# Kernel tuning notes

Hardware: AMD Instinct MI355X
Metric: run time of the kernel (lower is better)

## Reference

```python
import jax, jax.numpy as jnp
import numpy as np
from jax import lax

B, C, H, W = 4, 256, 64, 64
M = 8
CP = C // M  # 32 attention channels
KS = (3, 5, 7, 9)
EPS = 1e-5


def conv1x1(a, w, b):
    # a: [B,Ci,H,W], w: [Co,Ci], b: [Co]
    return jnp.einsum('bchw,oc->bohw', a, w) + b[None, :, None, None]


def _patches(a, k):
    # im2col with padding k//2, stride 1 (matches torch.nn.Unfold(k,1,k//2,1))
    pad = k // 2
    p = lax.conv_general_dilated_patches(a, (k, k), (1, 1), [(pad, pad), (pad, pad)])
    Bb, Cc = a.shape[0], a.shape[1]
    return p.reshape(Bb, Cc, k * k, a.shape[2], a.shape[3])  # [B,C',k^2,H,W]


def local_attn(km, qm, xm, k):
    # query is the center of each patch == qm itself (stride 1, pad k//2)
    kp = _patches(km, k)                                   # [B,C',k^2,H,W]
    scores = jnp.einsum('bckhw,bchw->bkhw', kp, qm)        # per-pixel k^2 logits
    attn = jax.nn.softmax(scores, axis=1)                  # softmax over window (dim=-2 in torch)
    xp = _patches(xm, k)                                   # [B,C',k^2,H,W]
    return jnp.einsum('bckhw,bkhw->bchw', xp, attn)        # [B,C',H,W]


def setup_inputs() -> dict:
    key = jax.random.key(0)
    ks = jax.random.split(key, 12)
    s_in = 1.0 / np.sqrt(C)
    s_out = 1.0 / np.sqrt(CP)
    return {
        'x': jax.random.normal(ks[0], (B, C, H, W), jnp.float32),
        'vessel': jax.random.uniform(ks[1], (B, 1, H, W), jnp.float32),
        'wk': jax.random.normal(ks[2], (CP, C), jnp.float32) * s_in,
        'bk': jnp.zeros((CP,), jnp.float32),
        'wq': jax.random.normal(ks[3], (CP, C), jnp.float32) * s_in,
        'bq': jnp.zeros((CP,), jnp.float32),
        'wx': jax.random.normal(ks[4], (CP, C), jnp.float32) * s_in,
        'bx': jnp.zeros((CP,), jnp.float32),
        'wf': jax.random.normal(ks[5], (C, CP), jnp.float32) * s_out,
        'bf': jnp.zeros((C,), jnp.float32),
        'gamma': jnp.ones((C,), jnp.float32),
        'beta': jnp.zeros((C,), jnp.float32),
    }


def reference(x, vessel, wk, bk, wq, bq, wx, bx, wf, bf, gamma, beta):
    km = conv1x1(x, wk, bk) * vessel   # key map masked by vessel
    qm = conv1x1(x, wq, bq)            # query map
    xm = conv1x1(x, wx, bx)            # value map
    pre = local_attn(km, qm, xm, KS[0])
    for k in KS[1:]:
        pre = pre + local_attn(km, qm, xm, k)
    y = conv1x1(pre, wf, bf)           # [B,C,H,W]
    # BatchNorm2d (training-mode batch stats)
    mean = y.mean(axis=(0, 2, 3), keepdims=True)
    var = y.var(axis=(0, 2, 3), keepdims=True)
    yn = (y - mean) * lax.rsqrt(var + EPS)
    return x + gamma[None, :, None, None] * yn + beta[None, :, None, None]
```

## Files before the change

### kernel.cpp

```cpp
#include <hip/hip_runtime.h>
#include <hip/hip_bf16.h>

typedef __hip_bfloat16 bf16;
typedef unsigned short u16;
typedef unsigned int u32;

typedef __bf16 bf16x8 __attribute__((ext_vector_type(8)));
typedef float f32x4 __attribute__((ext_vector_type(4)));

__device__ __forceinline__ float bf2f(bf16 v) { return __bfloat162float(v); }
__device__ __forceinline__ float us2f(u16 u) {
    union { u32 i; float f; } c; c.i = ((u32)u) << 16; return c.f;
}
__device__ __forceinline__ u16 f2u(float f) {
    union { bf16 b; u16 u; } c; c.b = __float2bfloat16(f); return c.u;
}

__global__ __launch_bounds__(256) void k_proj(
    const float* __restrict__ x, const float* __restrict__ vessel,
    const float* __restrict__ wk, const float* __restrict__ bk,
    const float* __restrict__ wq, const float* __restrict__ bq,
    const float* __restrict__ wx, const float* __restrict__ bx,
    bf16* __restrict__ km, bf16* __restrict__ qm, bf16* __restrict__ xm,
    float* __restrict__ partials)
{
    __shared__ u16 xs[64 * 264];
    __shared__ u16 wsh[48 * 264];
    const int tid = threadIdx.x;
    const int bid = blockIdx.x;
    const int nh = bid & 1;
    const int pt = bid >> 1;
    const int b  = pt >> 6;
    const int p0 = (pt & 63) * 64;

    if (bid < 64) {
#pragma unroll
        for (int i = 0; i < 5; ++i) {
            const int idx = tid + i * 256;
            if (idx < 1056) partials[bid * 1056 + idx] = 0.f;
        }
    }

#pragma unroll
    for (int i = 0; i < 16; ++i) {
        const int idx4 = tid + i * 256;
        const int ch = idx4 >> 4;
        const int px4 = (idx4 & 15) * 4;
        const float4 v = *(const float4*)&x[(b * 256 + ch) * 4096 + p0 + px4];
        xs[(px4 + 0) * 264 + ch] = f2u(v.x);
        xs[(px4 + 1) * 264 + ch] = f2u(v.y);
        xs[(px4 + 2) * 264 + ch] = f2u(v.z);
        xs[(px4 + 3) * 264 + ch] = f2u(v.w);
    }
#pragma unroll
    for (int i = 0; i < 12; ++i) {
        const int idx4 = tid + i * 256;
        const int o = idx4 >> 6;
        const int ch4 = (idx4 & 63) * 4;
        const int go = nh * 48 + o;
        const float* wp = (go < 32) ? wk : ((go < 64) ? wq : wx);
        const float4 v = *(const float4*)&wp[(go & 31) * 256 + ch4];
        wsh[o * 264 + ch4 + 0] = f2u(v.x);
        wsh[o * 264 + ch4 + 1] = f2u(v.y);
        wsh[o * 264 + ch4 + 2] = f2u(v.z);
        wsh[o * 264 + ch4 + 3] = f2u(v.w);
    }
    __syncthreads();

    const int w = tid >> 6;
    const int lane = tid & 63;
    const int lm = lane & 15, quad = lane >> 4;

    f32x4 acc0 = {0.f, 0.f, 0.f, 0.f};
    f32x4 acc1 = {0.f, 0.f, 0.f, 0.f};
    f32x4 acc2 = {0.f, 0.f, 0.f, 0.f};
#pragma unroll
    for (int kk = 0; kk < 8; ++kk) {
        const int k0 = kk * 32 + quad * 8;
        const bf16x8 a  = *(const bf16x8*)&xs[(w * 16 + lm) * 264 + k0];
        const bf16x8 b0 = *(const bf16x8*)&wsh[(0 + lm) * 264 + k0];
        const bf16x8 b1 = *(const bf16x8*)&wsh[(16 + lm) * 264 + k0];
        const bf16x8 b2 = *(const bf16x8*)&wsh[(32 + lm) * 264 + k0];
        acc0 = __builtin_amdgcn_mfma_f32_16x16x32_bf16(a, b0, acc0, 0, 0, 0);
        acc1 = __builtin_amdgcn_mfma_f32_16x16x32_bf16(a, b1, acc1, 0, 0, 0);
        acc2 = __builtin_amdgcn_mfma_f32_16x16x32_bf16(a, b2, acc2, 0, 0, 0);
    }
#pragma unroll
    for (int t = 0; t < 3; ++t) {
        const f32x4 acc = (t == 0) ? acc0 : ((t == 1) ? acc1 : acc2);
        const int go = nh * 48 + t * 16 + lm;
        const float* bs = (go < 32) ? bk : ((go < 64) ? bq : bx);
        const float bias = bs[go & 31];
        bf16* dst = (go < 32) ? km : ((go < 64) ? qm : xm);
#pragma unroll
        for (int rg = 0; rg < 4; ++rg) {
            const int px = p0 + w * 16 + quad * 4 + rg;
            float vv = acc[rg] + bias;
            if (go < 32) vv *= vessel[b * 4096 + px];
            dst[(b * 4096 + px) * 32 + (go & 31)] = __float2bfloat16(vv);
        }
    }
}

__global__ __launch_bounds__(256, 3) void k_attn(
    const bf16* __restrict__ km, const bf16* __restrict__ qm,
    const bf16* __restrict__ xm, bf16* __restrict__ pre,
    float* __restrict__ partials)
{
    __shared__ u16 kT[192 * 40];
    __shared__ u16 xTt[32 * 200];
    __shared__ float S[32 * 196];
    u16* P = kT;
    u16* preT = (u16*)S;

    const int tid = threadIdx.x;
    const int b = blockIdx.x >> 7;
    const int t128 = blockIdx.x & 127;
    const int h0 = (t128 >> 3) * 4;
    const int w0 = (t128 & 7) * 8;
    const u16* uk = (const u16*)km;
    const u16* ux = (const u16*)xm;
    const u16* uq = (const u16*)qm;
    const uint4 z4 = {0u, 0u, 0u, 0u};

#pragma unroll
    for (int i = 0; i < 3; ++i) {
        const int idx4 = tid + i * 256;
        const int pos = idx4 >> 2, c8 = idx4 & 3;
        const int gh = h0 - 4 + (pos >> 4), gw = w0 - 4 + (pos & 15);
        uint4 kv = z4, xv = z4;
        if (gh >= 0 && gh < 64 && gw >= 0 && gw < 64) {
            const int g = ((b << 12) + (gh << 6) + gw) * 32 + c8 * 8;
            kv = *(const uint4*)&uk[g];
            xv = *(const uint4*)&ux[g];
        }
        *(uint4*)&kT[pos * 40 + c8 * 8] = kv;
        const u16* xu = (const u16*)&xv;
#pragma unroll
        for (int t = 0; t < 8; ++t)
            xTt[(c8 * 8 + t) * 200 + pos] = xu[t];
    }
    __syncthreads();

    const int w = tid >> 6;
    const int lane = tid & 63;
    const int lm = lane & 15, quad = lane >> 4;

#pragma unroll
    for (int i = 0; i < 6; ++i) {
        const int t = w + i * 4;
        const int m = t / 12, n = t - m * 12;
        const int am = m * 16 + lm;
        const int qgh = h0 + (am >> 3), qgw = w0 + (am & 7);
        const bf16x8 a =
            *(const bf16x8*)&uq[(((b << 12) + (qgh << 6) + qgw) << 5) + quad * 8];
        const bf16x8 bb = *(const bf16x8*)&kT[(n * 16 + lm) * 40 + quad * 8];
        f32x4 acc = {0.f, 0.f, 0.f, 0.f};
        acc = __builtin_amdgcn_mfma_f32_16x16x32_bf16(a, bb, acc, 0, 0, 0);
#pragma unroll
        for (int rg = 0; rg < 4; ++rg)
            S[(m * 16 + quad * 4 + rg) * 196 + n * 16 + lm] = acc[rg];
    }
    __syncthreads();

    const int px = tid >> 3, cg = tid & 7;
    const int ty = px >> 3, tx = px & 7;
    float e[24];
    float Z3 = 0.f, Z5 = 0.f, Z7 = 0.f, Z9 = 0.f;
#pragma unroll
    for (int i = 0; i < 24; ++i) {
        const int pos = cg + 8 * i;
        const int hy = pos >> 4, hx = pos & 15;
        const int dy = hy - 4 - ty, dx = hx - 4 - tx;
        const int ady = dy < 0 ? -dy : dy, adx = dx < 0 ? -dx : dx;
        const int r = ady > adx ? ady : adx;
        const float s = S[px * 196 + pos];
        const float ev = (r <= 4) ? __expf(s) : 0.f;
        e[i] = ev;
        if (r <= 1) Z3 += ev;
        if (r <= 2) Z5 += ev;
        if (r <= 3) Z7 += ev;
        Z9 += ev;
    }
#pragma unroll
    for (int m = 1; m <= 4; m <<= 1) {
        Z3 += __shfl_xor(Z3, m);
        Z5 += __shfl_xor(Z5, m);
        Z7 += __shfl_xor(Z7, m);
        Z9 += __shfl_xor(Z9, m);
    }
    const float iZ3 = 1.f / Z3, iZ5 = 1.f / Z5, iZ7 = 1.f / Z7, iZ9 = 1.f / Z9;
#pragma unroll
    for (int i = 0; i < 24; ++i) {
        const int pos = cg + 8 * i;
        const int hy = pos >> 4, hx = pos & 15;
        const int dy = hy - 4 - ty, dx = hx - 4 - tx;
        const int ady = dy < 0 ? -dy : dy, adx = dx < 0 ? -dx : dx;
        const int r = ady > adx ? ady : adx;
        float coef = iZ9;
        if (r <= 1) coef += iZ3;
        if (r <= 2) coef += iZ5;
        if (r <= 3) coef += iZ7;
        P[px * 200 + pos] = f2u(e[i] * coef);
    }
    __syncthreads();

    const int m0 = w >> 1, n0 = w & 1;
    f32x4 acc = {0.f, 0.f, 0.f, 0.f};
#pragma unroll
    for (int kk = 0; kk < 6; ++kk) {
        const int k0 = kk * 32 + quad * 8;
        const bf16x8 a = *(const bf16x8*)&P[(m0 * 16 + lm) * 200 + k0];
        const bf16x8 bb = *(const bf16x8*)&xTt[(n0 * 16 + lm) * 200 + k0];
        acc = __builtin_amdgcn_mfma_f32_16x16x32_bf16(a, bb, acc, 0, 0, 0);
    }
#pragma unroll
    for (int rg = 0; rg < 4; ++rg) {
        const int pl = m0 * 16 + quad * 4 + rg;
        const int gh = h0 + (pl >> 3), gw = w0 + (pl & 7);
        pre[(((b << 12) + (gh << 6) + gw) << 5) + n0 * 16 + lm] =
            __float2bfloat16(acc[rg]);
        preT[(n0 * 16 + lm) * 40 + pl] = f2u(acc[rg]);
    }
    __syncthreads();

    const int it = w >> 1, jt = w & 1;
    if (w != 2) {
        const bf16x8 ca = *(const bf16x8*)&preT[(it * 16 + lm) * 40 + quad * 8];
        const bf16x8 cb = *(const bf16x8*)&preT[(jt * 16 + lm) * 40 + quad * 8];
        f32x4 cacc = {0.f, 0.f, 0.f, 0.f};
        cacc = __builtin_amdgcn_mfma_f32_16x16x32_bf16(ca, cb, cacc, 0, 0, 0);
        float* pslot = &partials[(blockIdx.x & 63) * 1056];
#pragma unroll
        for (int rg = 0; rg < 4; ++rg) {
            const int ii = it * 16 + quad * 4 + rg, jj = jt * 16 + lm;
            atomicAdd(&pslot[ii * 32 + jj], cacc[rg]);
        }
    }
    if (tid < 128) {
        float* pslot = &partials[(blockIdx.x & 63) * 1056];
        const int cc = tid >> 2, sg = tid & 3;
        float s = 0.f;
#pragma unroll
        for (int p = 0; p < 8; ++p) s += us2f(preT[cc * 40 + sg * 8 + p]);
        s += __shfl_xor(s, 1);
        s += __shfl_xor(s, 2);
        if (sg == 0) atomicAdd(&pslot[1024 + cc], s);
    }
}

__global__ __launch_bounds__(256) void k_stats(
    const float* __restrict__ partials, const float* __restrict__ wf,
    const float* __restrict__ gamma, const float* __restrict__ beta,
    float* __restrict__ Aout, float* __restrict__ Sout,
    u16* __restrict__ wfh, u16* __restrict__ wfl)
{
    __shared__ float cov[1024];
    __shared__ float mu[32];
    const int tid = threadIdx.x;
    float4 a = {0.f, 0.f, 0.f, 0.f};
    for (int blk = 0; blk < 64; ++blk) {
        const float4 p = *(const float4*)&partials[blk * 1056 + tid * 4];
        a.x += p.x; a.y += p.y; a.z += p.z; a.w += p.w;
    }
    *(float4*)&cov[tid * 4] = a;
    if (tid < 32) {
        float s = 0.f;
        for (int blk = 0; blk < 64; ++blk) s += partials[blk * 1056 + 1024 + tid];
        mu[tid] = s * (1.f / 16384.f);
    }
    __syncthreads();
    {
        const int fi = 16 + (tid >> 4), fj = tid & 15;
        cov[fi * 32 + fj] = cov[fj * 32 + fi];
    }
    __syncthreads();

    float wo[32];
#pragma unroll
    for (int c = 0; c < 32; ++c) wo[c] = wf[tid * 32 + c];

    __attribute__((aligned(16))) u16 hb[32];
    __attribute__((aligned(16))) u16 lb[32];
#pragma unroll
    for (int c = 0; c < 32; ++c) {
        const float v = wo[c];
        const u16 h = f2u(v);
        hb[c] = h;
        lb[c] = f2u(v - us2f(h));
    }
#pragma unroll
    for (int c8 = 0; c8 < 4; ++c8) {
        *(uint4*)&wfh[tid * 32 + c8 * 8] = *(const uint4*)&hb[c8 * 8];
        *(uint4*)&wfl[tid * 32 + c8 * 8] = *(const uint4*)&lb[c8 * 8];
    }

    float mv = 0.f;
#pragma unroll
    for (int c = 0; c < 32; ++c) mv += wo[c] * mu[c];
    float qacc = 0.f;
    for (int i2 = 0; i2 < 32; ++i2) {
        float t = 0.f;
#pragma unroll
        for (int j2 = 0; j2 < 32; ++j2) t += wo[j2] * cov[i2 * 32 + j2];
        qacc += wo[i2] * t;
    }
    const float var = qacc * (1.f / 16384.f) - mv * mv;
    const float A = gamma[tid] * rsqrtf(var + 1e-5f);
    Aout[tid] = A;
    Sout[tid] = beta[tid] - A * mv;
}

__global__ __launch_bounds__(256) void k_out(
    const bf16* __restrict__ pre, const u16* __restrict__ wfh,
    const u16* __restrict__ wfl, const float* __restrict__ x,
    const float* __restrict__ A, const float* __restrict__ S,
    float* __restrict__ out)
{
    __shared__ u16 wh[256 * 40];
    __shared__ u16 wl[256 * 40];
    __shared__ u16 pL[32 * 40];
    const int tid = threadIdx.x;
    const int gp0 = blockIdx.x * 32;
    const int b = gp0 >> 12, p0 = gp0 & 4095;

#pragma unroll
    for (int i = 0; i < 4; ++i) {
        const int idx = tid + i * 256;
        const int o = idx >> 2, c8 = idx & 3;
        *(uint4*)&wh[o * 40 + c8 * 8] = *(const uint4*)&wfh[o * 32 + c8 * 8];
        *(uint4*)&wl[o * 40 + c8 * 8] = *(const uint4*)&wfl[o * 32 + c8 * 8];
    }
    if (tid < 128) {
        const int px = tid >> 2, c8 = tid & 3;
        *(uint4*)&pL[px * 40 + c8 * 8] =
            *(const uint4*)&((const u16*)pre)[(gp0 + px) * 32 + c8 * 8];
    }
    __syncthreads();

    const int w = tid >> 6;
    const int lane = tid & 63;
    const int lm = lane & 15, quad = lane >> 4;

    bf16x8 pb[2];
    pb[0] = *(const bf16x8*)&pL[(0 + lm) * 40 + quad * 8];
    pb[1] = *(const bf16x8*)&pL[(16 + lm) * 40 + quad * 8];

    f32x4 acc[4][2];
#pragma unroll
    for (int mm = 0; mm < 4; ++mm) {
        const int orow = w * 64 + mm * 16 + lm;
        const bf16x8 ah = *(const bf16x8*)&wh[orow * 40 + quad * 8];
        const bf16x8 al = *(const bf16x8*)&wl[orow * 40 + quad * 8];
#pragma unroll
        for (int n = 0; n < 2; ++n) {
            f32x4 t = {0.f, 0.f, 0.f, 0.f};
            t = __builtin_amdgcn_mfma_f32_16x16x32_bf16(ah, pb[n], t, 0, 0, 0);
            acc[mm][n] =
                __builtin_amdgcn_mfma_f32_16x16x32_bf16(al, pb[n], t, 0, 0, 0);
        }
    }

#pragma unroll
    for (int mm = 0; mm < 4; ++mm) {
#pragma unroll
        for (int rg = 0; rg < 4; ++rg) {
            const int o = w * 64 + mm * 16 + quad * 4 + rg;
            const float Ao = A[o], So = S[o];
#pragma unroll
            for (int n = 0; n < 2; ++n) {
                const int ga = ((b << 8) + o) * 4096 + p0 + n * 16 + lm;
                out[ga] = x[ga] + Ao * acc[mm][n][rg] + So;
            }
        }
    }
}

extern "C" void kernel_launch(void* const* d_in, const int* in_sizes, int n_in,
                              void* d_out, int out_size, void* d_ws, size_t ws_size,
                              hipStream_t stream)
{
    (void)in_sizes; (void)n_in; (void)out_size; (void)ws_size;
    float* out = (float*)d_out;
    char* ws = (char*)d_ws;

    const float* x      = (const float*)d_in[0];
    const float* vessel = (const float*)d_in[1];
    const float* wk     = (const float*)d_in[2];
    const float* bk     = (const float*)d_in[3];
    const float* wq     = (const float*)d_in[4];
    const float* bq     = (const float*)d_in[5];
    const float* wx     = (const float*)d_in[6];
    const float* bx     = (const float*)d_in[7];
    const float* wf     = (const float*)d_in[8];
    const float* gamma  = (const float*)d_in[10];
    const float* beta   = (const float*)d_in[11];

    bf16* km  = (bf16*)(ws);
    bf16* qm  = (bf16*)(ws + 1048576);
    bf16* xm  = (bf16*)(ws + 2097152);
    bf16* pre = (bf16*)(ws + 3145728);
    float* partials = (float*)(ws + 4194304);
    float* Abuf     = (float*)(ws + 4464640);
    float* Sbuf     = (float*)(ws + 4465664);
    u16*   wfh      = (u16*)  (ws + 4466688);
    u16*   wfl      = (u16*)  (ws + 4483072);

    k_proj <<<512, 256, 0, stream>>>(x, vessel, wk, bk, wq, bq, wx, bx,
                                     km, qm, xm, partials);
    k_attn <<<512, 256, 0, stream>>>(km, qm, xm, pre, partials);
    k_stats<<<  1, 256, 0, stream>>>(partials, wf, gamma, beta, Abuf, Sbuf,
                                     wfh, wfl);
    k_out  <<<512, 256, 0, stream>>>(pre, wfh, wfl, x, Abuf, Sbuf, out);
}
```

Baseline: 122.3 us.

## Fold BatchNorm stats kernel into output kernel, recomputing per block

Removes the single-block k_stats launch and has every k_out block reduce the partials, build the covariance, compute per-channel scale and shift in shared memory, and split wf into bf16 hi/lo parts itself. This drops one kernel launch and the serial one-block stage between attention and output. In exchange every one of the 512 blocks re-reads all 64 partial slots (about 270KB each) and redoes the 32x32 quadratic form per channel, which adds redundant global traffic and ALU work. The variance now uses the hi+lo reconstruction of wf rather than the original fp32 weights.

```diff
diff --git a/kernel.cpp b/kernel.cpp
--- a/kernel.cpp
+++ b/kernel.cpp
@@ -249,92 +249,88 @@
     }
 }
 
-__global__ __launch_bounds__(256) void k_stats(
-    const float* __restrict__ partials, const float* __restrict__ wf,
-    const float* __restrict__ gamma, const float* __restrict__ beta,
-    float* __restrict__ Aout, float* __restrict__ Sout,
-    u16* __restrict__ wfh, u16* __restrict__ wfl)
-{
-    __shared__ float cov[1024];
-    __shared__ float mu[32];
-    const int tid = threadIdx.x;
-    float4 a = {0.f, 0.f, 0.f, 0.f};
-    for (int blk = 0; blk < 64; ++blk) {
-        const float4 p = *(const float4*)&partials[blk * 1056 + tid * 4];
-        a.x += p.x; a.y += p.y; a.z += p.z; a.w += p.w;
-    }
-    *(float4*)&cov[tid * 4] = a;
-    if (tid < 32) {
-        float s = 0.f;
-        for (int blk = 0; blk < 64; ++blk) s += partials[blk * 1056 + 1024 + tid];
-        mu[tid] = s * (1.f / 16384.f);
-    }
-    __syncthreads();
-    {
-        const int fi = 16 + (tid >> 4), fj = tid & 15;
-        cov[fi * 32 + fj] = cov[fj * 32 + fi];
-    }
-    __syncthreads();
-
-    float wo[32];
-#pragma unroll
-    for (int c = 0; c < 32; ++c) wo[c] = wf[tid * 32 + c];
-
-    __attribute__((aligned(16))) u16 hb[32];
-    __attribute__((aligned(16))) u16 lb[32];
-#pragma unroll
-    for (int c = 0; c < 32; ++c) {
-        const float v = wo[c];
-        const u16 h = f2u(v);
-        hb[c] = h;
-        lb[c] = f2u(v - us2f(h));
-    }
-#pragma unroll
-    for (int c8 = 0; c8 < 4; ++c8) {
-        *(uint4*)&wfh[tid * 32 + c8 * 8] = *(const uint4*)&hb[c8 * 8];
-        *(uint4*)&wfl[tid * 32 + c8 * 8] = *(const uint4*)&lb[c8 * 8];
-    }
-
-    float mv = 0.f;
-#pragma unroll
-    for (int c = 0; c < 32; ++c) mv += wo[c] * mu[c];
-    float qacc = 0.f;
-    for (int i2 = 0; i2 < 32; ++i2) {
-        float t = 0.f;
-#pragma unroll
-        for (int j2 = 0; j2 < 32; ++j2) t += wo[j2] * cov[i2 * 32 + j2];
-        qacc += wo[i2] * t;
-    }
-    const float var = qacc * (1.f / 16384.f) - mv * mv;
-    const float A = gamma[tid] * rsqrtf(var + 1e-5f);
-    Aout[tid] = A;
-    Sout[tid] = beta[tid] - A * mv;
-}
-
 __global__ __launch_bounds__(256) void k_out(
-    const bf16* __restrict__ pre, const u16* __restrict__ wfh,
-    const u16* __restrict__ wfl, const float* __restrict__ x,
-    const float* __restrict__ A, const float* __restrict__ S,
+    const bf16* __restrict__ pre, const float* __restrict__ wf,
+    const float* __restrict__ partials, const float* __restrict__ gamma,
+    const float* __restrict__ beta, const float* __restrict__ x,
     float* __restrict__ out)
 {
     __shared__ u16 wh[256 * 40];
     __shared__ u16 wl[256 * 40];
     __shared__ u16 pL[32 * 40];
+    __shared__ float cov[1024];
+    __shared__ float mu[32];
+    __shared__ float As[256];
+    __shared__ float Ss[256];
     const int tid = threadIdx.x;
     const int gp0 = blockIdx.x * 32;
     const int b = gp0 >> 12, p0 = gp0 & 4095;
 
 #pragma unroll
-    for (int i = 0; i < 4; ++i) {
+    for (int i = 0; i < 8; ++i) {
         const int idx = tid + i * 256;
-        const int o = idx >> 2, c8 = idx & 3;
-        *(uint4*)&wh[o * 40 + c8 * 8] = *(const uint4*)&wfh[o * 32 + c8 * 8];
-        *(uint4*)&wl[o * 40 + c8 * 8] = *(const uint4*)&wfl[o * 32 + c8 * 8];
+        const int o = idx >> 3, c4 = idx & 7;
+        const float4 v = *(const float4*)&wf[o * 32 + c4 * 4];
+        ushort4 hv, lv;
+        hv.x = f2u(v.x); lv.x = f2u(v.x - us2f(hv.x));
+        hv.y = f2u(v.y); lv.y = f2u(v.y - us2f(hv.y));
+        hv.z = f2u(v.z); lv.z = f2u(v.z - us2f(hv.z));
+        hv.w = f2u(v.w); lv.w = f2u(v.w - us2f(hv.w));
+        *(ushort4*)&wh[o * 40 + c4 * 4] = hv;
+        *(ushort4*)&wl[o * 40 + c4 * 4] = lv;
     }
     if (tid < 128) {
         const int px = tid >> 2, c8 = tid & 3;
         *(uint4*)&pL[px * 40 + c8 * 8] =
             *(const uint4*)&((const u16*)pre)[(gp0 + px) * 32 + c8 * 8];
+    }
+    {
+        float4 a4 = {0.f, 0.f, 0.f, 0.f};
+        for (int blk = 0; blk < 64; ++blk) {
+            const float4 p = *(const float4*)&partials[blk * 1056 + tid * 4];
+            a4.x += p.x; a4.y += p.y; a4.z += p.z; a4.w += p.w;
+        }
+        *(float4*)&cov[tid * 4] = a4;
+    }
+    if (tid < 32) {
+        float s = 0.f;
+        for (int blk = 0; blk < 64; ++blk) s += partials[blk * 1056 + 1024 + tid];
+        mu[tid] = s * (1.f / 16384.f);
+    }
+    __syncthreads();
+
+    {
+        const int fi = 16 + (tid >> 4), fj = tid & 15;
+        cov[fi * 32 + fj] = cov[fj * 32 + fi];
+    }
+    __syncthreads();
+
+    {
+        float wo[32];
+#pragma unroll
+        for (int c8 = 0; c8 < 4; ++c8) {
+            const uint4 hv = *(const uint4*)&wh[tid * 40 + c8 * 8];
+            const uint4 lv = *(const uint4*)&wl[tid * 40 + c8 * 8];
+            const u16* hp = (const u16*)&hv;
+            const u16* lp = (const u16*)&lv;
+#pragma unroll
+            for (int t = 0; t < 8; ++t)
+                wo[c8 * 8 + t] = us2f(hp[t]) + us2f(lp[t]);
+        }
+        float mv = 0.f;
+#pragma unroll
+        for (int c = 0; c < 32; ++c) mv += wo[c] * mu[c];
+        float qacc = 0.f;
+        for (int i2 = 0; i2 < 32; ++i2) {
+            float t = 0.f;
+#pragma unroll
+            for (int j2 = 0; j2 < 32; ++j2) t += wo[j2] * cov[i2 * 32 + j2];
+            qacc += wo[i2] * t;
+        }
+        const float var = qacc * (1.f / 16384.f) - mv * mv;
+        const float A = gamma[tid] * rsqrtf(var + 1e-5f);
+        As[tid] = A;
+        Ss[tid] = beta[tid] - A * mv;
     }
     __syncthreads();
 
@@ -366,7 +362,7 @@
 #pragma unroll
         for (int rg = 0; rg < 4; ++rg) {
             const int o = w * 64 + mm * 16 + quad * 4 + rg;
-            const float Ao = A[o], So = S[o];
+            const float Ao = As[o], So = Ss[o];
 #pragma unroll
             for (int n = 0; n < 2; ++n) {
                 const int ga = ((b << 8) + o) * 4096 + p0 + n * 16 + lm;
@@ -401,15 +397,9 @@
     bf16* xm  = (bf16*)(ws + 2097152);
     bf16* pre = (bf16*)(ws + 3145728);
     float* partials = (float*)(ws + 4194304);
-    float* Abuf     = (float*)(ws + 4464640);
-    float* Sbuf     = (float*)(ws + 4465664);
-    u16*   wfh      = (u16*)  (ws + 4466688);
-    u16*   wfl      = (u16*)  (ws + 4483072);
 
     k_proj <<<512, 256, 0, stream>>>(x, vessel, wk, bk, wq, bq, wx, bx,
                                      km, qm, xm, partials);
     k_attn <<<512, 256, 0, stream>>>(km, qm, xm, pre, partials);
-    k_stats<<<  1, 256, 0, stream>>>(partials, wf, gamma, beta, Abuf, Sbuf,
-                                     wfh, wfl);
-    k_out  <<<512, 256, 0, stream>>>(pre, wfh, wfl, x, Abuf, Sbuf, out);
-}
+    k_out  <<<512, 256, 0, stream>>>(pre, wf, partials, gamma, beta, x, out);
+}
```

New measurement: 120.2 us. Within noise of the previous version (-1.7%).
